# Kernel tuning notes

Measured on AMD Instinct MI355X. Metric: run time of the kernel, lower is better.

The kernel has to match this reference:

```python
import jax, jax.numpy as jnp
import numpy as np

H, DK, DV, SEG, D = 16, 64, 64, 512, 1024


def setup_inputs() -> dict:
    key = jax.random.key(0)
    ks = jax.random.split(key, 6)
    B, T = 2, 8192
    x = jax.random.normal(ks[0], (B, T, D), jnp.float32)
    Wq = jax.random.normal(ks[1], (H * DK, D), jnp.float32) * 0.02
    Wk = jax.random.normal(ks[2], (H * DK, D), jnp.float32) * 0.02
    Wv = jax.random.normal(ks[3], (H * DV, D), jnp.float32) * 0.02
    Wout = jax.random.normal(ks[4], (D, H * DV), jnp.float32) * 0.02
    betas = jax.random.normal(ks[5], (1, H, 1, DV), jnp.float32)
    return {"x": x, "Wq": Wq, "Wk": Wk, "Wv": Wv, "Wout": Wout, "betas": betas}


def reference(x, Wq, Wk, Wv, Wout, betas):
    B, T, _ = x.shape
    n_seg = T // SEG
    # Projections for the whole sequence, then PyTorch-style .view head split:
    # per segment, (B, SEG, H*dk).view(B, H, SEG, dk) is a raw row-major reshape.
    q = (x @ Wq.T).reshape(B, n_seg, H, SEG, DK)
    k = (x @ Wk.T).reshape(B, n_seg, H, SEG, DK)
    v = (x @ Wv.T).reshape(B, n_seg, H, SEG, DV)
    qs = jnp.moveaxis(q, 1, 0)  # (n_seg, B, H, SEG, DK)
    ks_ = jnp.moveaxis(k, 1, 0)
    vs = jnp.moveaxis(v, 1, 0)

    gate = jax.nn.sigmoid(betas)                 # (1, H, 1, DV)
    scale = 1.0 / jnp.sqrt(jnp.float32(DK))

    mem0 = jnp.zeros((B, H, DK, DV), x.dtype)
    # z broadcasts from (B,H,DV,1) to (B,H,DV,DK) on first update; start dense.
    z0 = jnp.zeros((B, H, DV, DK), x.dtype)

    def step(carry, seg):
        mem, z = carry
        q, k, v = seg
        sq = jax.nn.elu(q) + 1.0                 # (B,H,S,DK)
        sk = jax.nn.elu(k) + 1.0
        z = z + sk.sum(axis=-2, keepdims=True)   # (B,H,DV,DK) via broadcast
        scores = jnp.einsum('bhsd,bhtd->bhst', q, k) * scale
        att_dot = jnp.einsum('bhst,bhtv->bhsv', jax.nn.softmax(scores, axis=-1), v)
        att_mem = jnp.einsum('bhsd,bhdv->bhsv', sq, mem) / jnp.einsum('bhsd,bhdv->bhsv', sq, z)
        mem = mem + jnp.einsum('bhsd,bhsv->bhdv', sk, v)  # linear update (after att_mem)
        att = gate * att_mem + (1.0 - gate) * att_dot     # (B,H,S,DV)
        # PyTorch .view(B, SEG, H*DV) on (B,H,S,DV): raw reshape, no transpose.
        y = att.reshape(B, SEG, H * DV) @ Wout.T          # (B,SEG,D)
        return (mem, z), y

    (_, _), ys = jax.lax.scan(step, (mem0, z0), (qs, ks_, vs))
    out = jnp.moveaxis(ys, 0, 1).reshape(B, T, D)
    return out
```

## Files before the change

kernel.cpp:

```cpp
#include <hip/hip_runtime.h>


#define H_ 16
#define SEG_ 512
#define NSEG_ 16
#define B_ 2
#define T_ 8192
#define D_ 1024
#define BT_ 16384

#define NPROJ ((size_t)BT_ * D_)
#define NW ((size_t)D_ * D_)

__device__ unsigned short g_qb[NPROJ], g_kb[NPROJ], g_vb[NPROJ];
__device__ unsigned short g_xh[NPROJ];
__device__ unsigned short g_wqkv[3 * NW];
__device__ unsigned short g_ath[NPROJ], g_atl[NPROJ];
__device__ unsigned short g_woh[NW], g_wol[NW];
__device__ unsigned short g_vt[(size_t)512 * 64 * 512];
__device__ float g_M[(size_t)512 * 4096];
__device__ float g_z[(size_t)512 * 64];

typedef __attribute__((ext_vector_type(8))) short short8;
typedef __attribute__((ext_vector_type(8))) unsigned short ushort8;
typedef __attribute__((ext_vector_type(4))) float f32x4;

__device__ __forceinline__ float elu1(float x) {
    return x > 0.f ? x + 1.f : __expf(x);
}
__device__ __forceinline__ unsigned short f2bf(float x) {
    unsigned u = __float_as_uint(x);
    u += 0x7fffu + ((u >> 16) & 1u);
    return (unsigned short)(u >> 16);
}
__device__ __forceinline__ float bf2f(unsigned short h) {
    return __uint_as_float((unsigned)h << 16);
}
__device__ __forceinline__ void load_lds16(const unsigned short* g, unsigned short* l) {
    __builtin_amdgcn_global_load_lds(
        (const __attribute__((address_space(1))) unsigned int*)g,
        (__attribute__((address_space(3))) unsigned int*)l, 16, 0, 0);
}
__device__ __forceinline__ int sz8(int row, int blk) {
    return row * 64 + ((blk ^ (row & 7)) << 3);
}

__global__ __launch_bounds__(256) void prep_cast(
    const float* __restrict__ x, const float* __restrict__ Wq,
    const float* __restrict__ Wk, const float* __restrict__ Wv,
    const float* __restrict__ Wout,
    unsigned short* __restrict__ xh, unsigned short* __restrict__ wqkv,
    unsigned short* __restrict__ woh, unsigned short* __restrict__ wol)
{
    const int b = blockIdx.x;
    const int nXB = (int)(NPROJ / 1024);
    const int nWB = (int)(NW / 1024);
    if (b < nXB + 3 * nWB) {
        const float* in;
        unsigned short* out;
        int i;
        if (b < nXB) {
            in = x; out = xh; i = (b * 256 + threadIdx.x) * 4;
        } else {
            const int wsel = (b - nXB) / nWB;
            const int wb   = (b - nXB) % nWB;
            in  = wsel == 0 ? Wq : (wsel == 1 ? Wk : Wv);
            out = wqkv + (size_t)wsel * NW;
            i = (wb * 256 + threadIdx.x) * 4;
        }
        float4 v = *(const float4*)(in + i);
        ushort4 h;
        h.x = f2bf(v.x); h.y = f2bf(v.y); h.z = f2bf(v.z); h.w = f2bf(v.w);
        *(ushort4*)(out + i) = h;
    } else {
        const int wb = b - nXB - 3 * nWB;
        const int i = (wb * 256 + threadIdx.x) * 4;
        float4 v = *(const float4*)(Wout + i);
        ushort4 h, l;
        h.x = f2bf(v.x); l.x = f2bf(v.x - bf2f(h.x));
        h.y = f2bf(v.y); l.y = f2bf(v.y - bf2f(h.y));
        h.z = f2bf(v.z); l.z = f2bf(v.z - bf2f(h.z));
        h.w = f2bf(v.w); l.w = f2bf(v.w - bf2f(h.w));
        *(ushort4*)(woh + i) = h;
        *(ushort4*)(wol + i) = l;
    }
}


#define VMC(N) asm volatile("s_waitcnt vmcnt(" #N ")" ::: "memory")

#define STAGE_A(p, h, tt, u) \
    load_lds16(Aw + ((h) * 128 + (u) * 8) * 1024 + (tt) * 64, \
               &lds[(p) * 32768 + ((h) * 128 + w * 16 + (u) * 8) * 64])
#define STAGE_B(p, h, tt, u) \
    load_lds16(Bww + ((h) * 128 + (u) * 8) * 1024 + (tt) * 64, \
               &lds[(p) * 32768 + 16384 + ((h) * 128 + w * 16 + (u) * 8) * 64])
#define STAGE_AH(p, h, tt) do { STAGE_A(p, h, tt, 0); STAGE_A(p, h, tt, 1); } while (0)
#define STAGE_BH(p, h, tt) do { STAGE_B(p, h, tt, 0); STAGE_B(p, h, tt, 1); } while (0)

#define LDA(PBUF, MLO) do { \
    _Pragma("unroll") for (int m2 = 0; m2 < 4; ++m2) \
    _Pragma("unroll") for (int ks2 = 0; ks2 < 2; ++ks2) \
        a[m2][ks2] = *(const short8*)&lds[(PBUF) * 32768 + aoff[ks2] + ((MLO) + m2) * 1024]; \
} while (0)

#define LDB(PBUF) do { \
    _Pragma("unroll") for (int n2 = 0; n2 < 4; ++n2) \
    _Pragma("unroll") for (int ks2 = 0; ks2 < 2; ++ks2) \
        b[n2][ks2] = *(const short8*)&lds[(PBUF) * 32768 + boff[ks2] + n2 * 1024]; \
} while (0)

#define MFMA_QUAD(MLO, NLO) do { \
    _Pragma("unroll") for (int m2 = 0; m2 < 4; ++m2) \
    _Pragma("unroll") for (int n2 = 0; n2 < 2; ++n2) \
    _Pragma("unroll") for (int ks2 = 0; ks2 < 2; ++ks2) \
        acc[(MLO) + m2][(NLO) + n2] = __builtin_amdgcn_mfma_f32_16x16x32_bf16( \
            a[m2][ks2], b[(NLO) + n2][ks2], acc[(MLO) + m2][(NLO) + n2], 0, 0, 0); \
} while (0)

#define PH(MLO, NLO) do { \
    __builtin_amdgcn_s_barrier(); \
    asm volatile("s_waitcnt lgkmcnt(0)" ::: "memory"); \
    __builtin_amdgcn_sched_barrier(0); \
    __builtin_amdgcn_s_setprio(1); \
    MFMA_QUAD(MLO, NLO); \
    __builtin_amdgcn_s_setprio(0); \
    __builtin_amdgcn_sched_barrier(0); \
    __builtin_amdgcn_s_barrier(); \
} while (0)

__global__ __launch_bounds__(512, 2) void gemm_qkv8(
    const unsigned short* __restrict__ A, const unsigned short* __restrict__ Bw,
    unsigned short* __restrict__ Q, unsigned short* __restrict__ Kp,
    unsigned short* __restrict__ V)
{
    __shared__ unsigned short lds[65536];
    const int t = threadIdx.x, lane = t & 63, w = t >> 6;
    const int wave_m = w >> 2, wave_n = w & 3;

    const int bid = blockIdx.x;
    const int sb = (bid & 7) * 96 + (bid >> 3);
    const int mb = sb / 12, nb = sb % 12;
    const int m0 = mb * 256, n0 = nb * 256;

    const int lrow = lane >> 3;
    const int lcol = ((lane & 7) ^ lrow) * 8;
    const unsigned short* Aw  = A  + (size_t)(m0 + w * 16 + lrow) * 1024 + lcol;
    const unsigned short* Bww = Bw + (size_t)(n0 + w * 16 + lrow) * 1024 + lcol;

    const int fr = lane & 15, g4 = lane >> 4;
    int aoff[2], boff[2];
#pragma unroll
    for (int ks2 = 0; ks2 < 2; ++ks2) {
        aoff[ks2] = (wave_m * 128 + fr) * 64 + (((ks2 * 4 + g4) ^ (fr & 7)) * 8);
        boff[ks2] = 16384 + (wave_n * 64 + fr) * 64 + (((ks2 * 4 + g4) ^ (fr & 7)) * 8);
    }

    f32x4 acc[8][4];
#pragma unroll
    for (int i = 0; i < 8; ++i)
#pragma unroll
        for (int j = 0; j < 4; ++j) acc[i][j] = (f32x4)0.f;
    short8 a[4][2], b[4][2];

    STAGE_BH(0, 0, 0); STAGE_BH(0, 1, 0); STAGE_AH(0, 0, 0); STAGE_AH(0, 1, 0);
    STAGE_BH(1, 0, 1); STAGE_BH(1, 1, 1); STAGE_AH(1, 0, 1);
    VMC(6);
    __builtin_amdgcn_s_barrier();

#pragma unroll 1
    for (int it = 0; it < 7; ++it) {
        const int t1 = 2 * it + 1, t2 = 2 * it + 2, t3 = 2 * it + 3;
        LDB(0); LDA(0, 0);
        STAGE_AH(1, 1, t1);
        PH(0, 0);
        STAGE_BH(0, 0, t2);
        PH(0, 2);
        LDA(0, 4);
        STAGE_BH(0, 1, t2);
        PH(4, 0);
        STAGE_AH(0, 0, t2);
        VMC(6);
        PH(4, 2);
        LDB(1); LDA(1, 0);
        STAGE_AH(0, 1, t2);
        PH(0, 0);
        STAGE_BH(1, 0, t3);
        PH(0, 2);
        LDA(1, 4);
        STAGE_BH(1, 1, t3);
        PH(4, 0);
        STAGE_AH(1, 0, t3);
        VMC(6);
        PH(4, 2);
    }
    LDB(0); LDA(0, 0);
    STAGE_AH(1, 1, 15);
    PH(0, 0);
    PH(0, 2);
    LDA(0, 4);
    PH(4, 0);
    VMC(0);
    PH(4, 2);
    LDB(1); LDA(1, 0);
    PH(0, 0);
    PH(0, 2);
    LDA(1, 4);
    PH(4, 0);
    PH(4, 2);

    const int ccol = lane & 15, crow = (lane >> 4) * 4;
#pragma unroll
    for (int m = 0; m < 8; ++m)
#pragma unroll
        for (int n = 0; n < 4; ++n) {
            const int col = wave_n * 64 + n * 16 + ccol;
            const int cb = col >> 3, cl = col & 7;
#pragma unroll
            for (int r = 0; r < 4; ++r) {
                const int row = wave_m * 128 + m * 16 + crow + r;
                lds[row * 256 + ((cb ^ (row & 31)) << 3) + cl] = f2bf(acc[m][n][r]);
            }
        }
    __syncthreads();
    const int which = n0 >> 10, col0 = n0 & 1023;
    unsigned short* outp = which == 0 ? Q : (which == 1 ? Kp : V);
    const int orow = t >> 1, och = (t & 1) * 128;
    unsigned short* gp = outp + (size_t)(m0 + orow) * 1024 + col0 + och;
#pragma unroll
    for (int u = 0; u < 128; u += 8) {
        const int bo = (och + u) >> 3;
        *(ushort8*)(gp + u) = *(const ushort8*)&lds[orow * 256 + ((bo ^ (orow & 31)) << 3)];
    }
}


#define OSTG(p, arrp, aroff, tt, u) \
    load_lds16(arrp + (size_t)(u) * 16 * 1024 + (tt) * 32, \
               &lds[(p) * 32768 + (aroff) + (w * 32 + (u) * 16) * 32])
#define OUNIT(p, arrp, aroff, tt) do { OSTG(p, arrp, aroff, tt, 0); OSTG(p, arrp, aroff, tt, 1); } while (0)

#define OLDA(PBUF, MLO) do { \
    _Pragma("unroll") for (int m2 = 0; m2 < 4; ++m2) { \
        ah[m2] = *(const short8*)&lds[(PBUF) * 32768 +         ao + ((MLO) + m2) * 512]; \
        al[m2] = *(const short8*)&lds[(PBUF) * 32768 +  8192 + ao + ((MLO) + m2) * 512]; \
    } \
} while (0)

#define OLDB(PBUF) do { \
    _Pragma("unroll") for (int n2 = 0; n2 < 4; ++n2) { \
        bh[n2] = *(const short8*)&lds[(PBUF) * 32768 + 16384 + bo + n2 * 512]; \
        bl[n2] = *(const short8*)&lds[(PBUF) * 32768 + 24576 + bo + n2 * 512]; \
    } \
} while (0)

#define OQUAD(MLO, NLO) do { \
    _Pragma("unroll") for (int m2 = 0; m2 < 4; ++m2) \
    _Pragma("unroll") for (int n2 = 0; n2 < 2; ++n2) { \
        acc[(MLO) + m2][(NLO) + n2] = __builtin_amdgcn_mfma_f32_16x16x32_bf16( \
            ah[m2], bh[(NLO) + n2], acc[(MLO) + m2][(NLO) + n2], 0, 0, 0); \
        acc[(MLO) + m2][(NLO) + n2] = __builtin_amdgcn_mfma_f32_16x16x32_bf16( \
            al[m2], bh[(NLO) + n2], acc[(MLO) + m2][(NLO) + n2], 0, 0, 0); \
        acc[(MLO) + m2][(NLO) + n2] = __builtin_amdgcn_mfma_f32_16x16x32_bf16( \
            ah[m2], bl[(NLO) + n2], acc[(MLO) + m2][(NLO) + n2], 0, 0, 0); \
    } \
} while (0)

#define OPH(MLO, NLO) do { \
    __builtin_amdgcn_s_barrier(); \
    asm volatile("s_waitcnt lgkmcnt(0)" ::: "memory"); \
    __builtin_amdgcn_sched_barrier(0); \
    __builtin_amdgcn_s_setprio(1); \
    OQUAD(MLO, NLO); \
    __builtin_amdgcn_s_setprio(0); \
    __builtin_amdgcn_sched_barrier(0); \
    __builtin_amdgcn_s_barrier(); \
} while (0)

__global__ __launch_bounds__(512, 2) void gemm_bt8(
    const unsigned short* __restrict__ Ah, const unsigned short* __restrict__ Al,
    const unsigned short* __restrict__ Bh, const unsigned short* __restrict__ Bl,
    float* __restrict__ C)
{
    __shared__ unsigned short lds[65536];
    const int t = threadIdx.x, lane = t & 63, w = t >> 6;
    const int wave_m = w >> 2, wave_n = w & 3;

    const int bid = blockIdx.x;
    const int sb = (bid & 7) * 32 + (bid >> 3);
    const int m0 = (sb >> 2) * 256, n0 = (sb & 3) * 256;

    const int lrow = lane >> 2;
    const int lcol = ((lane & 3) ^ ((lane >> 3) & 3)) * 8;
    const unsigned short* Ahp = Ah + (size_t)(m0 + w * 32 + lrow) * 1024 + lcol;
    const unsigned short* Alp = Al + (size_t)(m0 + w * 32 + lrow) * 1024 + lcol;
    const unsigned short* Bhp = Bh + (size_t)(n0 + w * 32 + lrow) * 1024 + lcol;
    const unsigned short* Blp = Bl + (size_t)(n0 + w * 32 + lrow) * 1024 + lcol;

    const int fr = lane & 15, g4 = lane >> 4;
    const int xo = (g4 ^ ((fr >> 1) & 3)) * 8;
    const int ao = (wave_m * 128 + fr) * 32 + xo;
    const int bo = (wave_n * 64 + fr) * 32 + xo;

    f32x4 acc[8][4];
#pragma unroll
    for (int i = 0; i < 8; ++i)
#pragma unroll
        for (int j = 0; j < 4; ++j) acc[i][j] = (f32x4)0.f;
    short8 ah[4], al[4], bh[4], bl[4];

    OUNIT(0, Bhp, 16384, 0); OUNIT(0, Blp, 24576, 0); OUNIT(0, Ahp, 0, 0); OUNIT(0, Alp, 8192, 0);
    OUNIT(1, Bhp, 16384, 1); OUNIT(1, Blp, 24576, 1); OUNIT(1, Ahp, 0, 1);
    VMC(6);
    __builtin_amdgcn_s_barrier();

#pragma unroll 1
    for (int it = 0; it < 15; ++it) {
        const int t1 = 2 * it + 1, t2 = 2 * it + 2, t3 = 2 * it + 3;
        OLDB(0); OLDA(0, 0);
        OUNIT(1, Alp, 8192, t1);
        OPH(0, 0);
        OUNIT(0, Bhp, 16384, t2);
        OPH(0, 2);
        OLDA(0, 4);
        OUNIT(0, Blp, 24576, t2);
        OPH(4, 0);
        OUNIT(0, Ahp, 0, t2);
        VMC(6);
        OPH(4, 2);
        OLDB(1); OLDA(1, 0);
        OUNIT(0, Alp, 8192, t2);
        OPH(0, 0);
        OUNIT(1, Bhp, 16384, t3);
        OPH(0, 2);
        OLDA(1, 4);
        OUNIT(1, Blp, 24576, t3);
        OPH(4, 0);
        OUNIT(1, Ahp, 0, t3);
        VMC(6);
        OPH(4, 2);
    }
    OLDB(0); OLDA(0, 0);
    OUNIT(1, Alp, 8192, 31);
    OPH(0, 0);
    OPH(0, 2);
    OLDA(0, 4);
    OPH(4, 0);
    VMC(0);
    OPH(4, 2);
    OLDB(1); OLDA(1, 0);
    OPH(0, 0);
    OPH(0, 2);
    OLDA(1, 4);
    OPH(4, 0);
    OPH(4, 2);

    const int ccol = lane & 15, crow = (lane >> 4) * 4;
#pragma unroll
    for (int m = 0; m < 8; ++m)
#pragma unroll
        for (int n = 0; n < 4; ++n) {
            float* cp = C + (size_t)(m0 + wave_m * 128 + m * 16 + crow) * 1024
                          + (n0 + wave_n * 64 + n * 16 + ccol);
#pragma unroll
            for (int r = 0; r < 4; ++r) cp[(size_t)r * 1024] = acc[m][n][r];
        }
}

__global__ __launch_bounds__(256) void seg_stats(
    const unsigned short* __restrict__ kproj, const unsigned short* __restrict__ vproj,
    float* __restrict__ Mseg, float* __restrict__ zsum,
    unsigned short* __restrict__ vtg)
{
    __shared__ unsigned short sm_kh[64 * 64];
    __shared__ unsigned short sm_kl[64 * 64];
    __shared__ unsigned short sm_vt[64 * 64];
    const int idx = blockIdx.x;
    const int seg = idx & 15;
    const int bh  = idx >> 4;
    const int h   = bh & 15;
    const int b   = bh >> 4;
    const size_t base = ((size_t)b * T_ + (size_t)seg * SEG_ + (size_t)h * 32) * D_;
    const unsigned short* kt = kproj + base;
    const unsigned short* vt = vproj + base;
    const int t    = threadIdx.x;
    const int lane = t & 63;
    const int w    = t >> 6;
    const int c16  = lane & 15;
    const int g4   = lane >> 4;
    const int lr   = t >> 2;
    const int lc   = (t & 3) * 16;

    short8 bones;
#pragma unroll
    for (int j = 0; j < 8; ++j) bones[j] = (short)0x3F80;

    f32x4 acc[4];
#pragma unroll
    for (int nt = 0; nt < 4; ++nt) acc[nt] = (f32x4)0.f;
    f32x4 zacc = (f32x4)0.f;

    for (int c0 = 0; c0 < SEG_; c0 += 64) {
        __syncthreads();
        {
            const int row = c0 + lane;
            const unsigned short* kp = kt + (size_t)row * 64 + w * 16;
            const unsigned short* vp = vt + (size_t)row * 64 + w * 16;
            ushort8 k0 = *(const ushort8*)kp, k1 = *(const ushort8*)(kp + 8);
            ushort8 v0 = *(const ushort8*)vp, v1 = *(const ushort8*)(vp + 8);
            const int tb = lane >> 3, tl = lane & 7;
#pragma unroll
            for (int e = 0; e < 8; ++e) {
                const float f0 = elu1(bf2f(k0[e]));
                const unsigned short h0 = f2bf(f0), l0 = f2bf(f0 - bf2f(h0));
                const float f1 = elu1(bf2f(k1[e]));
                const unsigned short h1 = f2bf(f1), l1 = f2bf(f1 - bf2f(h1));
                const int a0 = sz8(w * 16 + e,     tb) + tl;
                const int a1 = sz8(w * 16 + 8 + e, tb) + tl;
                sm_kh[a0] = h0; sm_kl[a0] = l0; sm_vt[a0] = v0[e];
                sm_kh[a1] = h1; sm_kl[a1] = l1; sm_vt[a1] = v1[e];
            }
        }
        __syncthreads();
#pragma unroll
        for (int ks = 0; ks < 2; ++ks) {
            const short8 ahh = *(const short8*)&sm_kh[sz8(w * 16 + c16, ks * 4 + g4)];
            const short8 alo = *(const short8*)&sm_kl[sz8(w * 16 + c16, ks * 4 + g4)];
            zacc = __builtin_amdgcn_mfma_f32_16x16x32_bf16(ahh, bones, zacc, 0, 0, 0);
            zacc = __builtin_amdgcn_mfma_f32_16x16x32_bf16(alo, bones, zacc, 0, 0, 0);
#pragma unroll
            for (int nt = 0; nt < 4; ++nt) {
                const short8 bv = *(const short8*)&sm_vt[sz8(nt * 16 + c16, ks * 4 + g4)];
                acc[nt] = __builtin_amdgcn_mfma_f32_16x16x32_bf16(ahh, bv, acc[nt], 0, 0, 0);
                acc[nt] = __builtin_amdgcn_mfma_f32_16x16x32_bf16(alo, bv, acc[nt], 0, 0, 0);
            }
        }
        {
            unsigned short* vo = vtg + ((size_t)idx * 64 + lr) * 512 + c0 + lc;
            *(ushort8*)vo       = *(const ushort8*)&sm_vt[sz8(lr, lc >> 3)];
            *(ushort8*)(vo + 8) = *(const ushort8*)&sm_vt[sz8(lr, (lc >> 3) + 1)];
        }
    }
    float* Mout = Mseg + (size_t)idx * 4096;
#pragma unroll
    for (int nt = 0; nt < 4; ++nt)
#pragma unroll
        for (int r = 0; r < 4; ++r)
            Mout[(size_t)(w * 16 + g4 * 4 + r) * 64 + nt * 16 + c16] = acc[nt][r];
    if (c16 == 0) {
#pragma unroll
        for (int r = 0; r < 4; ++r)
            zsum[(size_t)idx * 64 + w * 16 + g4 * 4 + r] = zacc[r];
    }
}

__global__ __launch_bounds__(256) void prefix_scan(
    float* __restrict__ M, float* __restrict__ z)
{
    const int blk = blockIdx.x;
    const int bh  = blk >> 2, sl = blk & 3;
    const int t   = threadIdx.x;
    const size_t off = (size_t)bh * NSEG_ * 4096 + (size_t)sl * 1024 + (size_t)t * 4;
    float4 run = make_float4(0.f, 0.f, 0.f, 0.f);
    float runz = 0.f;
    for (int seg = 0; seg < NSEG_; ++seg) {
        const size_t o = off + (size_t)seg * 4096;
        float4 m = *(const float4*)(M + o);
        *(float4*)(M + o) = run;
        run.x += m.x; run.y += m.y; run.z += m.z; run.w += m.w;
        if (sl == 0 && t < 64) {
            const size_t oz = ((size_t)bh * NSEG_ + seg) * 64 + t;
            runz += z[oz];
            z[oz] = runz;
        }
    }
}

__global__ __launch_bounds__(256) void attn_mfma(
    const unsigned short* __restrict__ qproj, const unsigned short* __restrict__ kproj,
    const unsigned short* __restrict__ vtg, const float* __restrict__ memb,
    const float* __restrict__ Zaf, const float* __restrict__ betas,
    unsigned short* __restrict__ ath, unsigned short* __restrict__ atl)
{
    __shared__ unsigned short sm_k[64 * 64];
    __shared__ unsigned short sm_v[64 * 64];
    __shared__ unsigned short sm_p[64 * 64];
    __shared__ float Zsh[64], gsh[64];

    const int idx  = blockIdx.x;
    const int qc   = (idx >> 3) & 7;
    const int rest = (idx >> 6) * 8 + (idx & 7);
    const int bh   = rest >> 4;
    const int seg  = rest & 15;
    const int h    = bh & 15;
    const int b    = bh >> 4;
    const size_t base = ((size_t)b * T_ + (size_t)seg * SEG_ + (size_t)h * 32) * D_;

    const int t    = threadIdx.x;
    const int lane = t & 63;
    const int w    = t >> 6;
    const int c16  = lane & 15;
    const int g4   = lane >> 4;
    const int lr   = t >> 2;
    const int lc   = (t & 3) * 16;

    const unsigned short* qt = qproj + base + (size_t)qc * 4096;
    const unsigned short* kt = kproj + base;
    const unsigned short* vt = vtg + (size_t)rest * (64 * 512);
    const float* mb = memb + (size_t)rest * 4096;

    if (t < 64) {
        Zsh[t] = Zaf[(size_t)rest * 64 + t];
        gsh[t] = 1.f / (1.f + __expf(-betas[h * 64 + t]));
    }

    short8 qh[2], sqh[2];
    float rowsum = 0.f;
#pragma unroll
    for (int ks = 0; ks < 2; ++ks) {
        const unsigned short* qp = qt + (size_t)(w * 16 + c16) * 64 + g4 * 8 + ks * 32;
        ushort8 qv = *(const ushort8*)qp;
        short8 qf, sf;
#pragma unroll
        for (int j = 0; j < 8; ++j) {
            float e = elu1(bf2f(qv[j]));
            rowsum += e;
            qf[j] = (short)qv[j];
            sf[j] = (short)f2bf(e);
        }
        qh[ks] = qf; sqh[ks] = sf;
    }
    rowsum += __shfl_xor(rowsum, 16);
    rowsum += __shfl_xor(rowsum, 32);

    {
        const float* mp = mb + (size_t)lr * 64 + lc;
#pragma unroll
        for (int u = 0; u < 4; ++u) {
            float4 m4 = *(const float4*)(mp + u * 4);
            sm_p[sz8(lc + u * 4 + 0, lr >> 3) + (lr & 7)] = f2bf(m4.x);
            sm_p[sz8(lc + u * 4 + 1, lr >> 3) + (lr & 7)] = f2bf(m4.y);
            sm_p[sz8(lc + u * 4 + 2, lr >> 3) + (lr & 7)] = f2bf(m4.z);
            sm_p[sz8(lc + u * 4 + 3, lr >> 3) + (lr & 7)] = f2bf(m4.w);
        }
    }
    __syncthreads();

    f32x4 numf[4];
#pragma unroll
    for (int nf = 0; nf < 4; ++nf) numf[nf] = (f32x4)0.f;
#pragma unroll
    for (int ks = 0; ks < 2; ++ks)
#pragma unroll
        for (int nf = 0; nf < 4; ++nf) {
            short8 bm = *(const short8*)&sm_p[sz8(nf * 16 + c16, g4 + ks * 4)];
            numf[nf] = __builtin_amdgcn_mfma_f32_16x16x32_bf16(sqh[ks], bm, numf[nf], 0, 0, 0);
        }

    short8 bones;
#pragma unroll
    for (int j = 0; j < 8; ++j) bones[j] = (short)0x3F80;

    f32x4 o[4];
#pragma unroll
    for (int nf = 0; nf < 4; ++nf) o[nf] = (f32x4)0.f;
    float mrow[4] = {-1e30f, -1e30f, -1e30f, -1e30f};
    float lrow[4] = {0.f, 0.f, 0.f, 0.f};

    for (int kb = 0; kb < 8; ++kb) {
        __syncthreads();
        {
            const unsigned short* kp = kt + (size_t)(kb * 64 + lr) * 64 + lc;
            *(ushort8*)&sm_k[sz8(lr, lc >> 3)]       = *(const ushort8*)kp;
            *(ushort8*)&sm_k[sz8(lr, (lc >> 3) + 1)] = *(const ushort8*)(kp + 8);
            const unsigned short* vp = vt + (size_t)lr * 512 + kb * 64 + lc;
            *(ushort8*)&sm_v[sz8(lr, lc >> 3)]       = *(const ushort8*)vp;
            *(ushort8*)&sm_v[sz8(lr, (lc >> 3) + 1)] = *(const ushort8*)(vp + 8);
        }
        __syncthreads();

        f32x4 s[4];
#pragma unroll
        for (int nf = 0; nf < 4; ++nf) s[nf] = (f32x4)0.f;
#pragma unroll
        for (int ks = 0; ks < 2; ++ks)
#pragma unroll
            for (int nf = 0; nf < 4; ++nf) {
                short8 bk = *(const short8*)&sm_k[sz8(nf * 16 + c16, g4 + ks * 4)];
                s[nf] = __builtin_amdgcn_mfma_f32_16x16x32_bf16(qh[ks], bk, s[nf], 0, 0, 0);
            }
#pragma unroll
        for (int nf = 0; nf < 4; ++nf) s[nf] *= 0.125f;

        float pmax[4];
#pragma unroll
        for (int r = 0; r < 4; ++r)
            pmax[r] = fmaxf(fmaxf(s[0][r], s[1][r]), fmaxf(s[2][r], s[3][r]));
        const bool ok = pmax[0] <= mrow[0] + 8.f && pmax[1] <= mrow[1] + 8.f &&
                        pmax[2] <= mrow[2] + 8.f && pmax[3] <= mrow[3] + 8.f;
        if (!__all(ok)) {
#pragma unroll
            for (int r = 0; r < 4; ++r) {
                float mx = pmax[r];
                mx = fmaxf(mx, __shfl_xor(mx, 1));
                mx = fmaxf(mx, __shfl_xor(mx, 2));
                mx = fmaxf(mx, __shfl_xor(mx, 4));
                mx = fmaxf(mx, __shfl_xor(mx, 8));
                const float mnew = fmaxf(mrow[r], mx);
                const float corr = __expf(mrow[r] - mnew);
                mrow[r] = mnew;
                lrow[r] *= corr;
#pragma unroll
                for (int nf = 0; nf < 4; ++nf) o[nf][r] *= corr;
            }
        }
#pragma unroll
        for (int nf = 0; nf < 4; ++nf)
#pragma unroll
            for (int r = 0; r < 4; ++r) {
                s[nf][r] = __expf(s[nf][r] - mrow[r]);
                sm_p[sz8(w * 16 + g4 * 4 + r, nf * 2 + (c16 >> 3)) + (c16 & 7)] =
                    f2bf(s[nf][r]);
            }

        f32x4 psum = (f32x4)0.f;
#pragma unroll
        for (int ks = 0; ks < 2; ++ks) {
            short8 pa = *(const short8*)&sm_p[sz8(w * 16 + c16, g4 + ks * 4)];
            psum = __builtin_amdgcn_mfma_f32_16x16x32_bf16(pa, bones, psum, 0, 0, 0);
#pragma unroll
            for (int nf = 0; nf < 4; ++nf) {
                short8 bv = *(const short8*)&sm_v[sz8(nf * 16 + c16, g4 + ks * 4)];
                o[nf] = __builtin_amdgcn_mfma_f32_16x16x32_bf16(pa, bv, o[nf], 0, 0, 0);
            }
        }
#pragma unroll
        for (int r = 0; r < 4; ++r) lrow[r] += psum[r];
    }

    __syncthreads();

    float rs[4], invl[4];
#pragma unroll
    for (int r = 0; r < 4; ++r) {
        rs[r]   = __shfl(rowsum, (g4 << 2) + r);
        invl[r] = 1.f / lrow[r];
    }
#pragma unroll
    for (int nf = 0; nf < 4; ++nf) {
        const int col = nf * 16 + c16;
        const float Zc = Zsh[col], gc = gsh[col];
        const float izc = 1.f / Zc;
#pragma unroll
        for (int r = 0; r < 4; ++r) {
            const float adot = o[nf][r] * invl[r];
            const float amem = numf[nf][r] * izc / rs[r];
            const float res  = gc * amem + (1.f - gc) * adot;
            const unsigned short hv = f2bf(res);
            const unsigned short lv = f2bf(res - bf2f(hv));
            const int row = w * 16 + g4 * 4 + r;
            const int so  = sz8(row, nf * 2 + (c16 >> 3)) + (c16 & 7);
            sm_k[so] = hv;
            sm_v[so] = lv;
        }
    }
    __syncthreads();
    {
        const size_t ob = base + (size_t)(qc * 64 + lr) * 64 + lc;
        *(ushort8*)(ath + ob)     = *(const ushort8*)&sm_k[sz8(lr, lc >> 3)];
        *(ushort8*)(ath + ob + 8) = *(const ushort8*)&sm_k[sz8(lr, (lc >> 3) + 1)];
        *(ushort8*)(atl + ob)     = *(const ushort8*)&sm_v[sz8(lr, lc >> 3)];
        *(ushort8*)(atl + ob + 8) = *(const ushort8*)&sm_v[sz8(lr, (lc >> 3) + 1)];
    }
}

extern "C" void kernel_launch(void* const* d_in, const int* in_sizes, int n_in,
                              void* d_out, int out_size, void* d_ws, size_t ws_size,
                              hipStream_t stream) {
    const float* x     = (const float*)d_in[0];
    const float* Wq    = (const float*)d_in[1];
    const float* Wk    = (const float*)d_in[2];
    const float* Wv    = (const float*)d_in[3];
    const float* Wout  = (const float*)d_in[4];
    const float* betas = (const float*)d_in[5];
    float* out = (float*)d_out;
    (void)d_ws; (void)ws_size;

    float *M, *z;
    unsigned short *qb, *kb, *vb, *xh, *wqkv, *vt, *ath, *atl, *woh, *wol;
    hipGetSymbolAddress((void**)&qb,   HIP_SYMBOL(g_qb));
    hipGetSymbolAddress((void**)&kb,   HIP_SYMBOL(g_kb));
    hipGetSymbolAddress((void**)&vb,   HIP_SYMBOL(g_vb));
    hipGetSymbolAddress((void**)&xh,   HIP_SYMBOL(g_xh));
    hipGetSymbolAddress((void**)&wqkv, HIP_SYMBOL(g_wqkv));
    hipGetSymbolAddress((void**)&vt,   HIP_SYMBOL(g_vt));
    hipGetSymbolAddress((void**)&ath,  HIP_SYMBOL(g_ath));
    hipGetSymbolAddress((void**)&atl,  HIP_SYMBOL(g_atl));
    hipGetSymbolAddress((void**)&woh,  HIP_SYMBOL(g_woh));
    hipGetSymbolAddress((void**)&wol,  HIP_SYMBOL(g_wol));
    hipGetSymbolAddress((void**)&M,    HIP_SYMBOL(g_M));
    hipGetSymbolAddress((void**)&z,    HIP_SYMBOL(g_z));

    const int nXB = (int)(NPROJ / 1024), nWB = (int)(NW / 1024);
    prep_cast<<<nXB + 4 * nWB, 256, 0, stream>>>(x, Wq, Wk, Wv, Wout,
                                                 xh, wqkv, woh, wol);

    gemm_qkv8<<<dim3(768), 512, 0, stream>>>(xh, wqkv, qb, kb, vb);
    seg_stats<<<B_ * H_ * NSEG_, 256, 0, stream>>>(kb, vb, M, z, vt);
    prefix_scan<<<B_ * H_ * 4, 256, 0, stream>>>(M, z);
    attn_mfma<<<B_ * H_ * NSEG_ * 8, 256, 0, stream>>>(qb, kb, vt, M, z, betas, ath, atl);
    gemm_bt8<<<dim3(256), 512, 0, stream>>>(ath, atl, woh, wol, out);
}
```

Before: 485.8 us.

## Process whole segment per block with K/V staged once in LDS

The attention kernel now launches one 512-thread block per (batch, head, segment) instead of eight 256-thread blocks per segment. The whole segment's K and V tiles (8x64x64 each) plus the memory matrix are loaded into shared memory once, and the block loops over four 128-row query chunks. This removes the redundant K/V/M global reloads across query-chunk blocks and the per-kb-iteration syncs. In exchange it uses about 140KB of LDS per block and launches only 512 blocks, which reduces occupancy and parallelism. It also adds extra syncs for writing out the hi/lo results through one shared buffer.

```diff
diff --git a/kernel.cpp b/kernel.cpp
--- a/kernel.cpp
+++ b/kernel.cpp
@@ -476,20 +476,19 @@
     }
 }
 
-__global__ __launch_bounds__(256) void attn_mfma(
+__global__ __launch_bounds__(512) void attn_mfma(
     const unsigned short* __restrict__ qproj, const unsigned short* __restrict__ kproj,
     const unsigned short* __restrict__ vtg, const float* __restrict__ memb,
     const float* __restrict__ Zaf, const float* __restrict__ betas,
     unsigned short* __restrict__ ath, unsigned short* __restrict__ atl)
 {
-    __shared__ unsigned short sm_k[64 * 64];
-    __shared__ unsigned short sm_v[64 * 64];
-    __shared__ unsigned short sm_p[64 * 64];
+    __shared__ unsigned short smK[8 * 4096];
+    __shared__ unsigned short smV[8 * 4096];
+    __shared__ unsigned short smM[4096];
+    __shared__ unsigned short smP[128 * 64];
     __shared__ float Zsh[64], gsh[64];
 
-    const int idx  = blockIdx.x;
-    const int qc   = (idx >> 3) & 7;
-    const int rest = (idx >> 6) * 8 + (idx & 7);
+    const int rest = blockIdx.x;
     const int bh   = rest >> 4;
     const int seg  = rest & 15;
     const int h    = bh & 15;
@@ -501,10 +500,10 @@
     const int w    = t >> 6;
     const int c16  = lane & 15;
     const int g4   = lane >> 4;
-    const int lr   = t >> 2;
-    const int lc   = (t & 3) * 16;
-
-    const unsigned short* qt = qproj + base + (size_t)qc * 4096;
+    const int sr   = t >> 3;
+    const int sg   = t & 7;
+
+    const unsigned short* qt = qproj + base;
     const unsigned short* kt = kproj + base;
     const unsigned short* vt = vtg + (size_t)rest * (64 * 512);
     const float* mb = memb + (size_t)rest * 4096;
@@ -514,163 +513,173 @@
         gsh[t] = 1.f / (1.f + __expf(-betas[h * 64 + t]));
     }
 
-    short8 qh[2], sqh[2];
-    float rowsum = 0.f;
-#pragma unroll
-    for (int ks = 0; ks < 2; ++ks) {
-        const unsigned short* qp = qt + (size_t)(w * 16 + c16) * 64 + g4 * 8 + ks * 32;
-        ushort8 qv = *(const ushort8*)qp;
-        short8 qf, sf;
-#pragma unroll
-        for (int j = 0; j < 8; ++j) {
-            float e = elu1(bf2f(qv[j]));
-            rowsum += e;
-            qf[j] = (short)qv[j];
-            sf[j] = (short)f2bf(e);
-        }
-        qh[ks] = qf; sqh[ks] = sf;
-    }
-    rowsum += __shfl_xor(rowsum, 16);
-    rowsum += __shfl_xor(rowsum, 32);
-
     {
-        const float* mp = mb + (size_t)lr * 64 + lc;
-#pragma unroll
-        for (int u = 0; u < 4; ++u) {
+        const float* mp = mb + (size_t)sr * 64 + sg * 8;
+#pragma unroll
+        for (int u = 0; u < 2; ++u) {
             float4 m4 = *(const float4*)(mp + u * 4);
-            sm_p[sz8(lc + u * 4 + 0, lr >> 3) + (lr & 7)] = f2bf(m4.x);
-            sm_p[sz8(lc + u * 4 + 1, lr >> 3) + (lr & 7)] = f2bf(m4.y);
-            sm_p[sz8(lc + u * 4 + 2, lr >> 3) + (lr & 7)] = f2bf(m4.z);
-            sm_p[sz8(lc + u * 4 + 3, lr >> 3) + (lr & 7)] = f2bf(m4.w);
-        }
+            smM[sz8(sg * 8 + u * 4 + 0, sr >> 3) + (sr & 7)] = f2bf(m4.x);
+            smM[sz8(sg * 8 + u * 4 + 1, sr >> 3) + (sr & 7)] = f2bf(m4.y);
+            smM[sz8(sg * 8 + u * 4 + 2, sr >> 3) + (sr & 7)] = f2bf(m4.z);
+            smM[sz8(sg * 8 + u * 4 + 3, sr >> 3) + (sr & 7)] = f2bf(m4.w);
+        }
+    }
+#pragma unroll
+    for (int kb = 0; kb < 8; ++kb) {
+        *(ushort8*)&smK[kb * 4096 + sz8(sr, sg)] =
+            *(const ushort8*)(kt + (size_t)(kb * 64 + sr) * 64 + sg * 8);
+        *(ushort8*)&smV[kb * 4096 + sz8(sr, sg)] =
+            *(const ushort8*)(vt + (size_t)sr * 512 + kb * 64 + sg * 8);
     }
     __syncthreads();
 
-    f32x4 numf[4];
-#pragma unroll
-    for (int nf = 0; nf < 4; ++nf) numf[nf] = (f32x4)0.f;
-#pragma unroll
-    for (int ks = 0; ks < 2; ++ks)
+    short8 bones;
+#pragma unroll
+    for (int j = 0; j < 8; ++j) bones[j] = (short)0x3F80;
+
+#pragma unroll 1
+    for (int qc2 = 0; qc2 < 4; ++qc2) {
+        short8 qh[2], sqh[2];
+        float rowsum = 0.f;
+#pragma unroll
+        for (int ks = 0; ks < 2; ++ks) {
+            const unsigned short* qp =
+                qt + (size_t)(qc2 * 128 + w * 16 + c16) * 64 + g4 * 8 + ks * 32;
+            ushort8 qv = *(const ushort8*)qp;
+            short8 qf, sf;
+#pragma unroll
+            for (int j = 0; j < 8; ++j) {
+                float e = elu1(bf2f(qv[j]));
+                rowsum += e;
+                qf[j] = (short)qv[j];
+                sf[j] = (short)f2bf(e);
+            }
+            qh[ks] = qf; sqh[ks] = sf;
+        }
+        rowsum += __shfl_xor(rowsum, 16);
+        rowsum += __shfl_xor(rowsum, 32);
+
+        f32x4 numf[4];
+#pragma unroll
+        for (int nf = 0; nf < 4; ++nf) numf[nf] = (f32x4)0.f;
+#pragma unroll
+        for (int ks = 0; ks < 2; ++ks)
+#pragma unroll
+            for (int nf = 0; nf < 4; ++nf) {
+                short8 bm = *(const short8*)&smM[sz8(nf * 16 + c16, g4 + ks * 4)];
+                numf[nf] = __builtin_amdgcn_mfma_f32_16x16x32_bf16(sqh[ks], bm, numf[nf], 0, 0, 0);
+            }
+
+        f32x4 o[4];
+#pragma unroll
+        for (int nf = 0; nf < 4; ++nf) o[nf] = (f32x4)0.f;
+        float mrow[4] = {-1e30f, -1e30f, -1e30f, -1e30f};
+        float lrow[4] = {0.f, 0.f, 0.f, 0.f};
+
+#pragma unroll 1
+        for (int kb = 0; kb < 8; ++kb) {
+            f32x4 s[4];
+#pragma unroll
+            for (int nf = 0; nf < 4; ++nf) s[nf] = (f32x4)0.f;
+#pragma unroll
+            for (int ks = 0; ks < 2; ++ks)
+#pragma unroll
+                for (int nf = 0; nf < 4; ++nf) {
+                    short8 bk = *(const short8*)&smK[kb * 4096 + sz8(nf * 16 + c16, g4 + ks * 4)];
+                    s[nf] = __builtin_amdgcn_mfma_f32_16x16x32_bf16(qh[ks], bk, s[nf], 0, 0, 0);
+                }
+#pragma unroll
+            for (int nf = 0; nf < 4; ++nf) s[nf] *= 0.125f;
+
+            float pmax[4];
+#pragma unroll
+            for (int r = 0; r < 4; ++r)
+                pmax[r] = fmaxf(fmaxf(s[0][r], s[1][r]), fmaxf(s[2][r], s[3][r]));
+            const bool ok = pmax[0] <= mrow[0] + 8.f && pmax[1] <= mrow[1] + 8.f &&
+                            pmax[2] <= mrow[2] + 8.f && pmax[3] <= mrow[3] + 8.f;
+            if (!__all(ok)) {
+#pragma unroll
+                for (int r = 0; r < 4; ++r) {
+                    float mx = pmax[r];
+                    mx = fmaxf(mx, __shfl_xor(mx, 1));
+                    mx = fmaxf(mx, __shfl_xor(mx, 2));
+                    mx = fmaxf(mx, __shfl_xor(mx, 4));
+                    mx = fmaxf(mx, __shfl_xor(mx, 8));
+                    const float mnew = fmaxf(mrow[r], mx);
+                    const float corr = __expf(mrow[r] - mnew);
+                    mrow[r] = mnew;
+                    lrow[r] *= corr;
+#pragma unroll
+                    for (int nf = 0; nf < 4; ++nf) o[nf][r] *= corr;
+                }
+            }
+#pragma unroll
+            for (int nf = 0; nf < 4; ++nf)
+#pragma unroll
+                for (int r = 0; r < 4; ++r) {
+                    s[nf][r] = __expf(s[nf][r] - mrow[r]);
+                    smP[sz8(w * 16 + g4 * 4 + r, nf * 2 + (c16 >> 3)) + (c16 & 7)] =
+                        f2bf(s[nf][r]);
+                }
+
+            f32x4 psum = (f32x4)0.f;
+#pragma unroll
+            for (int ks = 0; ks < 2; ++ks) {
+                short8 pa = *(const short8*)&smP[sz8(w * 16 + c16, g4 + ks * 4)];
+                psum = __builtin_amdgcn_mfma_f32_16x16x32_bf16(pa, bones, psum, 0, 0, 0);
+#pragma unroll
+                for (int nf = 0; nf < 4; ++nf) {
+                    short8 bv = *(const short8*)&smV[kb * 4096 + sz8(nf * 16 + c16, g4 + ks * 4)];
+                    o[nf] = __builtin_amdgcn_mfma_f32_16x16x32_bf16(pa, bv, o[nf], 0, 0, 0);
+                }
+            }
+#pragma unroll
+            for (int r = 0; r < 4; ++r) lrow[r] += psum[r];
+        }
+
+        float rs[4], invl[4];
+#pragma unroll
+        for (int r = 0; r < 4; ++r) {
+            rs[r]   = __shfl(rowsum, (g4 << 2) + r);
+            invl[r] = 1.f / lrow[r];
+        }
+        float res[4][4];
 #pragma unroll
         for (int nf = 0; nf < 4; ++nf) {
-            short8 bm = *(const short8*)&sm_p[sz8(nf * 16 + c16, g4 + ks * 4)];
-            numf[nf] = __builtin_amdgcn_mfma_f32_16x16x32_bf16(sqh[ks], bm, numf[nf], 0, 0, 0);
-        }
-
-    short8 bones;
-#pragma unroll
-    for (int j = 0; j < 8; ++j) bones[j] = (short)0x3F80;
-
-    f32x4 o[4];
-#pragma unroll
-    for (int nf = 0; nf < 4; ++nf) o[nf] = (f32x4)0.f;
-    float mrow[4] = {-1e30f, -1e30f, -1e30f, -1e30f};
-    float lrow[4] = {0.f, 0.f, 0.f, 0.f};
-
-    for (int kb = 0; kb < 8; ++kb) {
+            const int col = nf * 16 + c16;
+            const float Zc = Zsh[col], gc = gsh[col];
+            const float izc = 1.f / Zc;
+#pragma unroll
+            for (int r = 0; r < 4; ++r) {
+                const float adot = o[nf][r] * invl[r];
+                const float amem = numf[nf][r] * izc / rs[r];
+                res[nf][r] = gc * amem + (1.f - gc) * adot;
+            }
+        }
+        const int orow = t >> 2, olc = (t & 3) * 16;
+        const size_t ob = base + (size_t)(qc2 * 128 + orow) * 64 + olc;
+#pragma unroll
+        for (int nf = 0; nf < 4; ++nf)
+#pragma unroll
+            for (int r = 0; r < 4; ++r)
+                smP[sz8(w * 16 + g4 * 4 + r, nf * 2 + (c16 >> 3)) + (c16 & 7)] =
+                    f2bf(res[nf][r]);
         __syncthreads();
-        {
-            const unsigned short* kp = kt + (size_t)(kb * 64 + lr) * 64 + lc;
-            *(ushort8*)&sm_k[sz8(lr, lc >> 3)]       = *(const ushort8*)kp;
-            *(ushort8*)&sm_k[sz8(lr, (lc >> 3) + 1)] = *(const ushort8*)(kp + 8);
-            const unsigned short* vp = vt + (size_t)lr * 512 + kb * 64 + lc;
-            *(ushort8*)&sm_v[sz8(lr, lc >> 3)]       = *(const ushort8*)vp;
-            *(ushort8*)&sm_v[sz8(lr, (lc >> 3) + 1)] = *(const ushort8*)(vp + 8);
-        }
+        *(ushort8*)(ath + ob)     = *(const ushort8*)&smP[sz8(orow, olc >> 3)];
+        *(ushort8*)(ath + ob + 8) = *(const ushort8*)&smP[sz8(orow, (olc >> 3) + 1)];
         __syncthreads();
-
-        f32x4 s[4];
-#pragma unroll
-        for (int nf = 0; nf < 4; ++nf) s[nf] = (f32x4)0.f;
-#pragma unroll
-        for (int ks = 0; ks < 2; ++ks)
-#pragma unroll
-            for (int nf = 0; nf < 4; ++nf) {
-                short8 bk = *(const short8*)&sm_k[sz8(nf * 16 + c16, g4 + ks * 4)];
-                s[nf] = __builtin_amdgcn_mfma_f32_16x16x32_bf16(qh[ks], bk, s[nf], 0, 0, 0);
-            }
-#pragma unroll
-        for (int nf = 0; nf < 4; ++nf) s[nf] *= 0.125f;
-
-        float pmax[4];
-#pragma unroll
-        for (int r = 0; r < 4; ++r)
-            pmax[r] = fmaxf(fmaxf(s[0][r], s[1][r]), fmaxf(s[2][r], s[3][r]));
-        const bool ok = pmax[0] <= mrow[0] + 8.f && pmax[1] <= mrow[1] + 8.f &&
-                        pmax[2] <= mrow[2] + 8.f && pmax[3] <= mrow[3] + 8.f;
-        if (!__all(ok)) {
+#pragma unroll
+        for (int nf = 0; nf < 4; ++nf)
 #pragma unroll
             for (int r = 0; r < 4; ++r) {
-                float mx = pmax[r];
-                mx = fmaxf(mx, __shfl_xor(mx, 1));
-                mx = fmaxf(mx, __shfl_xor(mx, 2));
-                mx = fmaxf(mx, __shfl_xor(mx, 4));
-                mx = fmaxf(mx, __shfl_xor(mx, 8));
-                const float mnew = fmaxf(mrow[r], mx);
-                const float corr = __expf(mrow[r] - mnew);
-                mrow[r] = mnew;
-                lrow[r] *= corr;
-#pragma unroll
-                for (int nf = 0; nf < 4; ++nf) o[nf][r] *= corr;
-            }
-        }
-#pragma unroll
-        for (int nf = 0; nf < 4; ++nf)
-#pragma unroll
-            for (int r = 0; r < 4; ++r) {
-                s[nf][r] = __expf(s[nf][r] - mrow[r]);
-                sm_p[sz8(w * 16 + g4 * 4 + r, nf * 2 + (c16 >> 3)) + (c16 & 7)] =
-                    f2bf(s[nf][r]);
-            }
-
-        f32x4 psum = (f32x4)0.f;
-#pragma unroll
-        for (int ks = 0; ks < 2; ++ks) {
-            short8 pa = *(const short8*)&sm_p[sz8(w * 16 + c16, g4 + ks * 4)];
-            psum = __builtin_amdgcn_mfma_f32_16x16x32_bf16(pa, bones, psum, 0, 0, 0);
-#pragma unroll
-            for (int nf = 0; nf < 4; ++nf) {
-                short8 bv = *(const short8*)&sm_v[sz8(nf * 16 + c16, g4 + ks * 4)];
-                o[nf] = __builtin_amdgcn_mfma_f32_16x16x32_bf16(pa, bv, o[nf], 0, 0, 0);
-            }
-        }
-#pragma unroll
-        for (int r = 0; r < 4; ++r) lrow[r] += psum[r];
-    }
-
-    __syncthreads();
-
-    float rs[4], invl[4];
-#pragma unroll
-    for (int r = 0; r < 4; ++r) {
-        rs[r]   = __shfl(rowsum, (g4 << 2) + r);
-        invl[r] = 1.f / lrow[r];
-    }
-#pragma unroll
-    for (int nf = 0; nf < 4; ++nf) {
-        const int col = nf * 16 + c16;
-        const float Zc = Zsh[col], gc = gsh[col];
-        const float izc = 1.f / Zc;
-#pragma unroll
-        for (int r = 0; r < 4; ++r) {
-            const float adot = o[nf][r] * invl[r];
-            const float amem = numf[nf][r] * izc / rs[r];
-            const float res  = gc * amem + (1.f - gc) * adot;
-            const unsigned short hv = f2bf(res);
-            const unsigned short lv = f2bf(res - bf2f(hv));
-            const int row = w * 16 + g4 * 4 + r;
-            const int so  = sz8(row, nf * 2 + (c16 >> 3)) + (c16 & 7);
-            sm_k[so] = hv;
-            sm_v[so] = lv;
-        }
-    }
-    __syncthreads();
-    {
-        const size_t ob = base + (size_t)(qc * 64 + lr) * 64 + lc;
-        *(ushort8*)(ath + ob)     = *(const ushort8*)&sm_k[sz8(lr, lc >> 3)];
-        *(ushort8*)(ath + ob + 8) = *(const ushort8*)&sm_k[sz8(lr, (lc >> 3) + 1)];
-        *(ushort8*)(atl + ob)     = *(const ushort8*)&sm_v[sz8(lr, lc >> 3)];
-        *(ushort8*)(atl + ob + 8) = *(const ushort8*)&sm_v[sz8(lr, (lc >> 3) + 1)];
+                const unsigned short hv = f2bf(res[nf][r]);
+                smP[sz8(w * 16 + g4 * 4 + r, nf * 2 + (c16 >> 3)) + (c16 & 7)] =
+                    f2bf(res[nf][r] - bf2f(hv));
+            }
+        __syncthreads();
+        *(ushort8*)(atl + ob)     = *(const ushort8*)&smP[sz8(orow, olc >> 3)];
+        *(ushort8*)(atl + ob + 8) = *(const ushort8*)&smP[sz8(orow, (olc >> 3) + 1)];
+        __syncthreads();
     }
 }
 
@@ -708,6 +717,6 @@
     gemm_qkv8<<<dim3(768), 512, 0, stream>>>(xh, wqkv, qb, kb, vb);
     seg_stats<<<B_ * H_ * NSEG_, 256, 0, stream>>>(kb, vb, M, z, vt);
     prefix_scan<<<B_ * H_ * 4, 256, 0, stream>>>(M, z);
-    attn_mfma<<<B_ * H_ * NSEG_ * 8, 256, 0, stream>>>(qb, kb, vt, M, z, betas, ath, atl);
+    attn_mfma<<<B_ * H_ * NSEG_, 512, 0, stream>>>(qb, kb, vt, M, z, betas, ath, atl);
     gemm_bt8<<<dim3(256), 512, 0, stream>>>(ath, atl, woh, wol, out);
 }
```

Result: no change. 483.7 us (-0.4%).
